# Kernel tuning notes

Measured on AMD Instinct MI355X. Metric: run time of the kernel, lower is better.

## Reference

```python
import jax, jax.numpy as jnp
import numpy as np

R, I, O = 100000, 512, 512  # nodes, input_dim, output_dim (= k of top-k)


def setup_inputs() -> dict:
    key = jax.random.key(0)
    ks = jax.random.split(key, 12)
    s = 0.05
    return {
        "inputs": jax.random.normal(ks[0], (R, I), dtype=jnp.float32),
        "hist": jax.random.normal(ks[1], (I, O), dtype=jnp.float32),
        "mask": jnp.zeros((R, 1), dtype=jnp.float32),
        "scorer": jax.random.normal(ks[2], (I, 1), dtype=jnp.float32) * s,
        "Wu": jax.random.normal(ks[3], (I, I), dtype=jnp.float32) * s,
        "Uu": jax.random.normal(ks[4], (I, I), dtype=jnp.float32) * s,
        "bu": jnp.zeros((I, O), dtype=jnp.float32),
        "Wr": jax.random.normal(ks[5], (I, I), dtype=jnp.float32) * s,
        "Ur": jax.random.normal(ks[6], (I, I), dtype=jnp.float32) * s,
        "br": jnp.zeros((I, O), dtype=jnp.float32),
        "Wh": jax.random.normal(ks[7], (I, I), dtype=jnp.float32) * s,
        "Uh": jax.random.normal(ks[8], (I, I), dtype=jnp.float32) * s,
        "bh": jnp.zeros((I, O), dtype=jnp.float32),
    }


def _topk(inputs, mask, scorer, k):
    # scores: (R,) = X @ p / ||p|| + mask
    norm = jnp.sqrt(jnp.sum(scorer * scorer)) + 1e-12
    scores = (inputs @ scorer)[:, 0] / norm + mask[:, 0]
    vals, idx = jax.lax.top_k(scores, k)            # (k,), (k,)
    # gather top-k rows, weight by tanh(score), transpose -> (I, k)
    return (inputs[idx] * jnp.tanh(vals)[:, None]).T


def _gate(x, h, W, U, b, act):
    return act(W @ x + U @ h + b)


def reference(inputs, hist, mask, scorer, Wu, Uu, bu, Wr, Ur, br, Wh, Uh, bh):
    x_topk = _topk(inputs, mask, scorer, O)          # (I, O)
    update = _gate(x_topk, hist, Wu, Uu, bu, jax.nn.sigmoid)
    reset = _gate(x_topk, hist, Wr, Ur, br, jax.nn.sigmoid)
    h_cap = _gate(x_topk, reset * hist, Wh, Uh, bh, jnp.tanh)
    return (1.0 - update) * hist + update * h_cap    # (I, O)
```

## Files before the change

### kernel.cpp

```cpp
#include <hip/hip_runtime.h>

#define R_NODES 100000
#define I_DIM 512
#define K_SEL 512

#define OFF_NORM   0
#define OFF_GHIST  256
#define OFF_KEYS   8704
#define OFF_SELIDX 408832
#define OFF_SELW   410880
#define OFF_XT     413696
#define OFF_HT     (OFF_XT + 524288)
#define OFF_W6     (OFF_HT + 524288)
#define OFF_U      (OFF_W6 + 6 * 524288)
#define OFF_RHT    (OFF_U + 1048576)

typedef __attribute__((ext_vector_type(8))) short bf16x8;
typedef __attribute__((ext_vector_type(4))) float f32x4;

__device__ __forceinline__ float sigf(float x) { return 1.0f / (1.0f + __expf(-x)); }
__device__ __forceinline__ unsigned short bfr(float x) {
  unsigned int u = __float_as_uint(x);
  u += 0x7FFFu + ((u >> 16) & 1u);
  return (unsigned short)(u >> 16);
}
#define LDS_SWZ(row, bytecol) ((((row) * 64) + (bytecol)) ^ (((row) & 7) << 4))

__global__ __launch_bounds__(256) void k_norm(const float* __restrict__ scorer,
                                              float* __restrict__ inv_norm,
                                              unsigned int* __restrict__ ghist) {
  __shared__ float red[256];
  int t = threadIdx.x;
  for (int b = t; b < 2048; b += 256) ghist[b] = 0u;
  float v0 = scorer[t], v1 = scorer[t + 256];
  red[t] = v0 * v0 + v1 * v1;
  __syncthreads();
  for (int s = 128; s > 0; s >>= 1) {
    if (t < s) red[t] += red[t + s];
    __syncthreads();
  }
  if (t == 0) inv_norm[0] = 1.0f / (sqrtf(red[0]) + 1e-12f);
}

__global__ __launch_bounds__(256) void k_scores(const float* __restrict__ inputs,
                                                const float* __restrict__ scorer,
                                                const float* __restrict__ mask,
                                                const float* __restrict__ inv_norm,
                                                unsigned int* __restrict__ keys) {
  const int wave = threadIdx.x >> 6;
  const int lane = threadIdx.x & 63;
  const int row = blockIdx.x * 4 + wave;
  const float4* rp = (const float4*)(inputs + (size_t)row * I_DIM);
  const float4* sp = (const float4*)scorer;
  float4 a0 = rp[lane], a1 = rp[lane + 64];
  float4 s0 = sp[lane], s1 = sp[lane + 64];
  float dot = a0.x * s0.x + a0.y * s0.y + a0.z * s0.z + a0.w * s0.w
            + a1.x * s1.x + a1.y * s1.y + a1.z * s1.z + a1.w * s1.w;
#pragma unroll
  for (int off = 32; off >= 1; off >>= 1) dot += __shfl_down(dot, off);
  if (lane == 0) {
    float score = dot * inv_norm[0] + mask[row];
    unsigned int u = __float_as_uint(score);
    keys[row] = (u & 0x80000000u) ? ~u : (u | 0x80000000u);
  }
}

__global__ __launch_bounds__(256) void k_hist1(const unsigned int* __restrict__ keys,
                                               unsigned int* __restrict__ ghist) {
  __shared__ unsigned int h[2048];
  int t = threadIdx.x;
  for (int b = t; b < 2048; b += 256) h[b] = 0u;
  __syncthreads();
  int per = (R_NODES + gridDim.x - 1) / gridDim.x;
  int start = blockIdx.x * per;
  int end = start + per;
  if (end > R_NODES) end = R_NODES;
  for (int r = start + t; r < end; r += 256) atomicAdd(&h[keys[r] >> 21], 1u);
  __syncthreads();
  for (int b = t; b < 2048; b += 256) {
    unsigned int v = h[b];
    if (v) atomicAdd(&ghist[b], v);
  }
}

#define SUFFIX_SCAN()                                                         \
  for (int off = 1; off < 2048; off <<= 1) {                                  \
    unsigned int v0 = (t + off < 2048) ? hist[t + off] : 0u;                  \
    unsigned int v1 = (t + 1024 + off < 2048) ? hist[t + 1024 + off] : 0u;    \
    __syncthreads();                                                          \
    hist[t] += v0;                                                            \
    hist[t + 1024] += v1;                                                     \
    __syncthreads();                                                          \
  }

#define FIND_BIN(needv)                                                       \
  {                                                                           \
    for (int q = 0; q < 2; ++q) {                                             \
      int b = t + q * 1024;                                                   \
      unsigned int s_here = hist[b];                                          \
      unsigned int s_next = (b < 2047) ? hist[b + 1] : 0u;                    \
      if (s_here >= (needv) && s_next < (needv)) {                            \
        sh_bin = (unsigned int)b;                                             \
        sh_above = s_next;                                                    \
      }                                                                       \
    }                                                                         \
    __syncthreads();                                                          \
  }

__global__ __launch_bounds__(1024) void k_select(const unsigned int* __restrict__ keys,
                                                 const unsigned int* __restrict__ ghist,
                                                 int* __restrict__ sel_idx,
                                                 float* __restrict__ sel_w) {
  __shared__ unsigned int hist[2048];
  __shared__ unsigned long long cand[2048];
  __shared__ unsigned int sh_bin, sh_above, sh_cnt;
  const int t = threadIdx.x;

  unsigned int need = K_SEL;
  hist[t] = ghist[t];
  hist[t + 1024] = ghist[t + 1024];
  __syncthreads();
  SUFFIX_SCAN();
  FIND_BIN(need);
  unsigned int b1 = sh_bin;
  need -= sh_above;
  __syncthreads();

  hist[t] = 0u;
  hist[t + 1024] = 0u;
  __syncthreads();
  for (int r = t; r < R_NODES; r += 1024) {
    unsigned int k2 = keys[r];
    if ((k2 >> 21) == b1) atomicAdd(&hist[(k2 >> 10) & 0x7FFu], 1u);
  }
  __syncthreads();
  SUFFIX_SCAN();
  FIND_BIN(need);
  unsigned int b2 = sh_bin;
  unsigned int T = ((b1 << 11) | b2) << 10;

  if (t == 0) sh_cnt = 0u;
  __syncthreads();
  for (int r = t; r < R_NODES; r += 1024) {
    unsigned int k2 = keys[r];
    if (k2 >= T) {
      unsigned int p = atomicAdd(&sh_cnt, 1u);
      if (p < 2048u)
        cand[p] = ((unsigned long long)k2 << 32) |
                  (unsigned long long)(0xFFFFFFFFu - (unsigned int)r);
    }
  }
  __syncthreads();
  unsigned int cnt = sh_cnt > 2048u ? 2048u : sh_cnt;
  for (int p = t; p < 2048; p += 1024)
    if ((unsigned int)p >= cnt) cand[p] = 0ULL;
  __syncthreads();

  for (int ks = 2; ks <= 2048; ks <<= 1) {
    for (int js = ks >> 1; js > 0; js >>= 1) {
      for (int i = t; i < 2048; i += 1024) {
        int ixj = i ^ js;
        if (ixj > i) {
          unsigned long long x = cand[i], y = cand[ixj];
          bool up = ((i & ks) == 0);
          if (up ? (x > y) : (x < y)) {
            cand[i] = y;
            cand[ixj] = x;
          }
        }
      }
      __syncthreads();
    }
  }

  for (int j = t; j < K_SEL; j += 1024) {
    unsigned long long c = cand[2047 - j];
    unsigned int key = (unsigned int)(c >> 32);
    unsigned int ridx = 0xFFFFFFFFu - (unsigned int)(c & 0xFFFFFFFFull);
    unsigned int ub = (key & 0x80000000u) ? (key ^ 0x80000000u) : ~key;
    float val = __uint_as_float(ub);
    sel_idx[j] = (int)ridx;
    sel_w[j] = tanhf(val);
  }
}

__global__ __launch_bounds__(256) void k_cvt(
    const float* __restrict__ Wu, const float* __restrict__ Uu,
    const float* __restrict__ Wr, const float* __restrict__ Ur,
    const float* __restrict__ Wh, const float* __restrict__ Uh,
    const float* __restrict__ hist,
    unsigned short* __restrict__ bW,
    unsigned short* __restrict__ bHt) {
  const int t = threadIdx.x;
  const int y = blockIdx.y;
  if (y < 6) {
    const float* srcs[6] = {Wu, Uu, Wr, Ur, Wh, Uh};
    const float* src = srcs[y];
    unsigned short* dst = bW + (size_t)y * (I_DIM * I_DIM);
    int idx4 = blockIdx.x * 256 + t;
    float4 v = ((const float4*)src)[idx4];
    ushort4 o;
    o.x = bfr(v.x); o.y = bfr(v.y); o.z = bfr(v.z); o.w = bfr(v.w);
    ((ushort4*)dst)[idx4] = o;
  } else {
    __shared__ float tile[32][33];
    const int ti = blockIdx.x >> 4;
    const int tj = blockIdx.x & 15;
    const int r = t >> 3;
    const int cq = (t & 7) * 4;
    float4 v = *(const float4*)&hist[(ti * 32 + r) * I_DIM + tj * 32 + cq];
    tile[r][cq + 0] = v.x; tile[r][cq + 1] = v.y;
    tile[r][cq + 2] = v.z; tile[r][cq + 3] = v.w;
    __syncthreads();
    ushort4 o;
    o.x = bfr(tile[cq + 0][r]);
    o.y = bfr(tile[cq + 1][r]);
    o.z = bfr(tile[cq + 2][r]);
    o.w = bfr(tile[cq + 3][r]);
    *(ushort4*)&bHt[(tj * 32 + r) * I_DIM + ti * 32 + cq] = o;
  }
}

__global__ __launch_bounds__(256) void k_build_xt(const float* __restrict__ inputs,
                                                  const int* __restrict__ sel_idx,
                                                  const float* __restrict__ sel_w,
                                                  unsigned short* __restrict__ bXt) {
  const int j = blockIdx.x;
  const int c = threadIdx.x;
  const int row = sel_idx[j];
  const float w = sel_w[j];
  float2 v = *(const float2*)&inputs[(size_t)row * I_DIM + c * 2];
  ushort2 o;
  o.x = bfr(v.x * w);
  o.y = bfr(v.y * w);
  *(ushort2*)&bXt[(size_t)j * I_DIM + c * 2] = o;
}

__device__ __forceinline__ void gemm64_dual(
    const unsigned short* __restrict__ A1, const unsigned short* __restrict__ A2,
    const unsigned short* __restrict__ B1t, const unsigned short* __restrict__ B2t,
    int i0, int j0, char* smem, f32x4 acc[2][2]) {
  const int t = threadIdx.x;
  const int w = t >> 6, l = t & 63;
  const int wm = w >> 1, wn = w & 1;
  const int lr = l & 15, lh = l >> 4;
  char* sA1 = smem;
  char* sA2 = smem + 4096;
  char* sB1 = smem + 8192;
  char* sB2 = smem + 12288;
  const int srow = t >> 2;
  const int kc = t & 3;
  const int sbyte = LDS_SWZ(srow, kc * 16);

  for (int ks = 0; ks < I_DIM / 32; ++ks) {
    const size_t ga = (size_t)(i0 + srow) * I_DIM + ks * 32 + kc * 8;
    const size_t gb = (size_t)(j0 + srow) * I_DIM + ks * 32 + kc * 8;
    uint4 va1 = *(const uint4*)(A1 + ga);
    uint4 va2 = *(const uint4*)(A2 + ga);
    uint4 vb1 = *(const uint4*)(B1t + gb);
    uint4 vb2 = *(const uint4*)(B2t + gb);
    __syncthreads();
    *(uint4*)(sA1 + sbyte) = va1;
    *(uint4*)(sA2 + sbyte) = va2;
    *(uint4*)(sB1 + sbyte) = vb1;
    *(uint4*)(sB2 + sbyte) = vb2;
    __syncthreads();
    bf16x8 a1[2], a2[2], b1[2], b2[2];
#pragma unroll
    for (int mf = 0; mf < 2; ++mf) {
      int rowA = wm * 32 + mf * 16 + lr;
      int off = LDS_SWZ(rowA, lh * 16);
      a1[mf] = *(const bf16x8*)(sA1 + off);
      a2[mf] = *(const bf16x8*)(sA2 + off);
    }
#pragma unroll
    for (int nf = 0; nf < 2; ++nf) {
      int rowB = wn * 32 + nf * 16 + lr;
      int off = LDS_SWZ(rowB, lh * 16);
      b1[nf] = *(const bf16x8*)(sB1 + off);
      b2[nf] = *(const bf16x8*)(sB2 + off);
    }
#pragma unroll
    for (int mf = 0; mf < 2; ++mf)
#pragma unroll
      for (int nf = 0; nf < 2; ++nf) {
        acc[mf][nf] = __builtin_amdgcn_mfma_f32_16x16x32_bf16(a1[mf], b1[nf], acc[mf][nf], 0, 0, 0);
        acc[mf][nf] = __builtin_amdgcn_mfma_f32_16x16x32_bf16(a2[mf], b2[nf], acc[mf][nf], 0, 0, 0);
      }
  }
}

__global__ __launch_bounds__(256) void k_gates_mfma(
    const unsigned short* __restrict__ bW, const unsigned short* __restrict__ bXt,
    const unsigned short* __restrict__ bHt,
    const float* __restrict__ bu, const float* __restrict__ br,
    const float* __restrict__ hist,
    float* __restrict__ U, unsigned short* __restrict__ bRHt) {
  __shared__ char smem[16384];
  const int i0 = blockIdx.y * 64, j0 = blockIdx.x * 64;
  const int z = blockIdx.z;
  const unsigned short* A1 = bW + (size_t)(z ? 2 : 0) * (I_DIM * I_DIM);
  const unsigned short* A2 = bW + (size_t)(z ? 3 : 1) * (I_DIM * I_DIM);
  f32x4 acc[2][2];
#pragma unroll
  for (int mf = 0; mf < 2; ++mf)
#pragma unroll
    for (int nf = 0; nf < 2; ++nf) acc[mf][nf] = (f32x4){0.f, 0.f, 0.f, 0.f};
  gemm64_dual(A1, A2, bXt, bHt, i0, j0, smem, acc);

  const int t = threadIdx.x;
  const int w = t >> 6, l = t & 63;
  const int wm = w >> 1, wn = w & 1;
  const int lr = l & 15, lh = l >> 4;
  const float* bias = z ? br : bu;
#pragma unroll
  for (int mf = 0; mf < 2; ++mf)
#pragma unroll
    for (int nf = 0; nf < 2; ++nf)
#pragma unroll
      for (int q = 0; q < 4; ++q) {
        int row = i0 + wm * 32 + mf * 16 + lh * 4 + q;
        int col = j0 + wn * 32 + nf * 16 + lr;
        int o = row * I_DIM + col;
        float g = sigf(acc[mf][nf][q] + bias[o]);
        if (z == 0) {
          U[o] = g;
        } else {
          bRHt[(size_t)col * I_DIM + row] = bfr(g * hist[o]);
        }
      }
}

__global__ __launch_bounds__(256) void k_final_mfma(
    const unsigned short* __restrict__ bW, const unsigned short* __restrict__ bXt,
    const unsigned short* __restrict__ bRHt,
    const float* __restrict__ bh, const float* __restrict__ U,
    const float* __restrict__ hist, float* __restrict__ out) {
  __shared__ char smem[16384];
  const int i0 = blockIdx.y * 64, j0 = blockIdx.x * 64;
  const unsigned short* A1 = bW + (size_t)4 * (I_DIM * I_DIM);
  const unsigned short* A2 = bW + (size_t)5 * (I_DIM * I_DIM);
  f32x4 acc[2][2];
#pragma unroll
  for (int mf = 0; mf < 2; ++mf)
#pragma unroll
    for (int nf = 0; nf < 2; ++nf) acc[mf][nf] = (f32x4){0.f, 0.f, 0.f, 0.f};
  gemm64_dual(A1, A2, bXt, bRHt, i0, j0, smem, acc);

  const int t = threadIdx.x;
  const int w = t >> 6, l = t & 63;
  const int wm = w >> 1, wn = w & 1;
  const int lr = l & 15, lh = l >> 4;
#pragma unroll
  for (int mf = 0; mf < 2; ++mf)
#pragma unroll
    for (int nf = 0; nf < 2; ++nf)
#pragma unroll
      for (int q = 0; q < 4; ++q) {
        int row = i0 + wm * 32 + mf * 16 + lh * 4 + q;
        int col = j0 + wn * 32 + nf * 16 + lr;
        int o = row * I_DIM + col;
        float hc = tanhf(acc[mf][nf][q] + bh[o]);
        float uu = U[o];
        out[o] = (1.f - uu) * hist[o] + uu * hc;
      }
}

extern "C" void kernel_launch(void* const* d_in, const int* in_sizes, int n_in,
                              void* d_out, int out_size, void* d_ws, size_t ws_size,
                              hipStream_t stream) {
  const float* inputs = (const float*)d_in[0];
  const float* hist   = (const float*)d_in[1];
  const float* mask   = (const float*)d_in[2];
  const float* scorer = (const float*)d_in[3];
  const float* Wu = (const float*)d_in[4];
  const float* Uu = (const float*)d_in[5];
  const float* bu = (const float*)d_in[6];
  const float* Wr = (const float*)d_in[7];
  const float* Ur = (const float*)d_in[8];
  const float* br = (const float*)d_in[9];
  const float* Wh = (const float*)d_in[10];
  const float* Uh = (const float*)d_in[11];
  const float* bh = (const float*)d_in[12];
  float* out = (float*)d_out;

  char* ws = (char*)d_ws;
  float* inv_norm = (float*)(ws + OFF_NORM);
  unsigned int* ghist = (unsigned int*)(ws + OFF_GHIST);
  unsigned int* keys = (unsigned int*)(ws + OFF_KEYS);
  int* sel_idx = (int*)(ws + OFF_SELIDX);
  float* sel_w = (float*)(ws + OFF_SELW);
  unsigned short* bXt = (unsigned short*)(ws + OFF_XT);
  unsigned short* bHt = (unsigned short*)(ws + OFF_HT);
  unsigned short* bW  = (unsigned short*)(ws + OFF_W6);
  float* U = (float*)(ws + OFF_U);
  unsigned short* bRHt = (unsigned short*)(ws + OFF_RHT);

  k_cvt<<<dim3(256, 7), 256, 0, stream>>>(Wu, Uu, Wr, Ur, Wh, Uh, hist, bW, bHt);
  k_norm<<<1, 256, 0, stream>>>(scorer, inv_norm, ghist);
  k_scores<<<R_NODES / 4, 256, 0, stream>>>(inputs, scorer, mask, inv_norm, keys);
  k_hist1<<<64, 256, 0, stream>>>(keys, ghist);
  k_select<<<1, 1024, 0, stream>>>(keys, ghist, sel_idx, sel_w);
  k_build_xt<<<512, 256, 0, stream>>>(inputs, sel_idx, sel_w, bXt);
  k_gates_mfma<<<dim3(8, 8, 2), 256, 0, stream>>>(bW, bXt, bHt, bu, br, hist, U, bRHt);
  k_final_mfma<<<dim3(8, 8), 256, 0, stream>>>(bW, bXt, bRHt, bh, U, hist, out);
}
```

Measured before the change: 421.8 us.

## Drop second radix pass in top-k select and fold norm kernel into convert

The single-block select kernel no longer builds a second-level histogram. It collects every key in the first-level threshold bin into the candidate buffer and bitonic-sorts 1024 entries instead of 2048 when the candidate count allows it. The separate norm/histogram-clear kernel is merged into the conversion kernel as an extra grid row, which removes one launch. The risk is that if more than 2048 keys share the top bin, candidates are truncated and the selection becomes incorrect. The extra grid row also launches 255 blocks that exit immediately.

```diff
diff --git a/kernel.cpp b/kernel.cpp
--- a/kernel.cpp
+++ b/kernel.cpp
@@ -25,22 +25,6 @@
   return (unsigned short)(u >> 16);
 }
 #define LDS_SWZ(row, bytecol) ((((row) * 64) + (bytecol)) ^ (((row) & 7) << 4))
-
-__global__ __launch_bounds__(256) void k_norm(const float* __restrict__ scorer,
-                                              float* __restrict__ inv_norm,
-                                              unsigned int* __restrict__ ghist) {
-  __shared__ float red[256];
-  int t = threadIdx.x;
-  for (int b = t; b < 2048; b += 256) ghist[b] = 0u;
-  float v0 = scorer[t], v1 = scorer[t + 256];
-  red[t] = v0 * v0 + v1 * v1;
-  __syncthreads();
-  for (int s = 128; s > 0; s >>= 1) {
-    if (t < s) red[t] += red[t + s];
-    __syncthreads();
-  }
-  if (t == 0) inv_norm[0] = 1.0f / (sqrtf(red[0]) + 1e-12f);
-}
 
 __global__ __launch_bounds__(256) void k_scores(const float* __restrict__ inputs,
                                                 const float* __restrict__ scorer,
@@ -101,7 +85,6 @@
       unsigned int s_next = (b < 2047) ? hist[b + 1] : 0u;                    \
       if (s_here >= (needv) && s_next < (needv)) {                            \
         sh_bin = (unsigned int)b;                                             \
-        sh_above = s_next;                                                    \
       }                                                                       \
     }                                                                         \
     __syncthreads();                                                          \
@@ -113,37 +96,22 @@
                                                  float* __restrict__ sel_w) {
   __shared__ unsigned int hist[2048];
   __shared__ unsigned long long cand[2048];
-  __shared__ unsigned int sh_bin, sh_above, sh_cnt;
-  const int t = threadIdx.x;
-
-  unsigned int need = K_SEL;
+  __shared__ unsigned int sh_bin, sh_cnt;
+  const int t = threadIdx.x;
+
   hist[t] = ghist[t];
   hist[t + 1024] = ghist[t + 1024];
   __syncthreads();
   SUFFIX_SCAN();
-  FIND_BIN(need);
+  FIND_BIN(K_SEL);
   unsigned int b1 = sh_bin;
-  need -= sh_above;
-  __syncthreads();
-
-  hist[t] = 0u;
-  hist[t + 1024] = 0u;
-  __syncthreads();
+  if (t == 0) sh_cnt = 0u;
+  __syncthreads();
+
+  const unsigned int kmin = b1 << 21;
   for (int r = t; r < R_NODES; r += 1024) {
     unsigned int k2 = keys[r];
-    if ((k2 >> 21) == b1) atomicAdd(&hist[(k2 >> 10) & 0x7FFu], 1u);
-  }
-  __syncthreads();
-  SUFFIX_SCAN();
-  FIND_BIN(need);
-  unsigned int b2 = sh_bin;
-  unsigned int T = ((b1 << 11) | b2) << 10;
-
-  if (t == 0) sh_cnt = 0u;
-  __syncthreads();
-  for (int r = t; r < R_NODES; r += 1024) {
-    unsigned int k2 = keys[r];
-    if (k2 >= T) {
+    if (k2 >= kmin) {
       unsigned int p = atomicAdd(&sh_cnt, 1u);
       if (p < 2048u)
         cand[p] = ((unsigned long long)k2 << 32) |
@@ -151,14 +119,15 @@
     }
   }
   __syncthreads();
-  unsigned int cnt = sh_cnt > 2048u ? 2048u : sh_cnt;
-  for (int p = t; p < 2048; p += 1024)
+  const unsigned int cnt = sh_cnt > 2048u ? 2048u : sh_cnt;
+  const int nsort = (cnt <= 1024u) ? 1024 : 2048;
+  for (int p = t; p < nsort; p += 1024)
     if ((unsigned int)p >= cnt) cand[p] = 0ULL;
   __syncthreads();
 
-  for (int ks = 2; ks <= 2048; ks <<= 1) {
+  for (int ks = 2; ks <= nsort; ks <<= 1) {
     for (int js = ks >> 1; js > 0; js >>= 1) {
-      for (int i = t; i < 2048; i += 1024) {
+      for (int i = t; i < nsort; i += 1024) {
         int ixj = i ^ js;
         if (ixj > i) {
           unsigned long long x = cand[i], y = cand[ixj];
@@ -174,7 +143,7 @@
   }
 
   for (int j = t; j < K_SEL; j += 1024) {
-    unsigned long long c = cand[2047 - j];
+    unsigned long long c = cand[nsort - 1 - j];
     unsigned int key = (unsigned int)(c >> 32);
     unsigned int ridx = 0xFFFFFFFFu - (unsigned int)(c & 0xFFFFFFFFull);
     unsigned int ub = (key & 0x80000000u) ? (key ^ 0x80000000u) : ~key;
@@ -189,8 +158,11 @@
     const float* __restrict__ Wr, const float* __restrict__ Ur,
     const float* __restrict__ Wh, const float* __restrict__ Uh,
     const float* __restrict__ hist,
+    const float* __restrict__ scorer,
     unsigned short* __restrict__ bW,
-    unsigned short* __restrict__ bHt) {
+    unsigned short* __restrict__ bHt,
+    float* __restrict__ inv_norm,
+    unsigned int* __restrict__ ghist) {
   const int t = threadIdx.x;
   const int y = blockIdx.y;
   if (y < 6) {
@@ -202,7 +174,7 @@
     ushort4 o;
     o.x = bfr(v.x); o.y = bfr(v.y); o.z = bfr(v.z); o.w = bfr(v.w);
     ((ushort4*)dst)[idx4] = o;
-  } else {
+  } else if (y == 6) {
     __shared__ float tile[32][33];
     const int ti = blockIdx.x >> 4;
     const int tj = blockIdx.x & 15;
@@ -218,6 +190,18 @@
     o.z = bfr(tile[cq + 2][r]);
     o.w = bfr(tile[cq + 3][r]);
     *(ushort4*)&bHt[(tj * 32 + r) * I_DIM + ti * 32 + cq] = o;
+  } else {
+    if (blockIdx.x != 0) return;
+    __shared__ float red[256];
+    for (int b = t; b < 2048; b += 256) ghist[b] = 0u;
+    float v0 = scorer[t], v1 = scorer[t + 256];
+    red[t] = v0 * v0 + v1 * v1;
+    __syncthreads();
+    for (int s = 128; s > 0; s >>= 1) {
+      if (t < s) red[t] += red[t + s];
+      __syncthreads();
+    }
+    if (t == 0) inv_norm[0] = 1.0f / (sqrtf(red[0]) + 1e-12f);
   }
 }
 
@@ -396,8 +380,8 @@
   float* U = (float*)(ws + OFF_U);
   unsigned short* bRHt = (unsigned short*)(ws + OFF_RHT);
 
-  k_cvt<<<dim3(256, 7), 256, 0, stream>>>(Wu, Uu, Wr, Ur, Wh, Uh, hist, bW, bHt);
-  k_norm<<<1, 256, 0, stream>>>(scorer, inv_norm, ghist);
+  k_cvt<<<dim3(256, 8), 256, 0, stream>>>(Wu, Uu, Wr, Ur, Wh, Uh, hist, scorer,
+                                          bW, bHt, inv_norm, ghist);
   k_scores<<<R_NODES / 4, 256, 0, stream>>>(inputs, scorer, mask, inv_norm, keys);
   k_hist1<<<64, 256, 0, stream>>>(keys, ghist);
   k_select<<<1, 1024, 0, stream>>>(keys, ghist, sel_idx, sel_w);
```

Measured after the change: 389.5 us. 7.7% less time.
